# Kernel optimization log

Hardware: AMD Instinct MI355X
Metric: run time of the kernel (lower is better)

The kernel has to match this reference:

```python
import jax, jax.numpy as jnp
import numpy as np

B, L, H, LAB = 64, 128, 512, 128

def setup_inputs() -> dict:
    key = jax.random.key(0)
    ks = jax.random.split(key, 8)
    s = 1.0 / np.sqrt(H)  # PyTorch LSTM/Linear uniform bound as a std-ish scale
    return {
        "x": jax.random.normal(ks[0], (B, L, 2 * H), jnp.float32),
        "hi": jax.random.normal(ks[1], (B, L, 2 * H), jnp.float32),
        "W_ih": jax.random.normal(ks[2], (4 * H, 5 * H), jnp.float32) * s,
        "W_hh": jax.random.normal(ks[3], (4 * H, H), jnp.float32) * s,
        "b_ih": jax.random.normal(ks[4], (4 * H,), jnp.float32) * s,
        "b_hh": jax.random.normal(ks[5], (4 * H,), jnp.float32) * s,
        "W_fc": jax.random.normal(ks[6], (LAB, H), jnp.float32) * s,
        "b_fc": jax.random.normal(ks[7], (LAB,), jnp.float32) * s,
    }

def _cell(xi, h, c, W_ih, W_hh, b_ih, b_hh):
    # PyTorch LSTMCell math, gate order: input, forget, cell(g), output
    gates = xi @ W_ih.T + b_ih + h @ W_hh.T + b_hh  # [4H]
    i, f, g, o = jnp.split(gates, 4)
    i = jax.nn.sigmoid(i); f = jax.nn.sigmoid(f); o = jax.nn.sigmoid(o)
    g = jnp.tanh(g)
    c = f * c + i * g
    h = o * jnp.tanh(c)
    return h, c

def reference(x, hi, W_ih, W_hh, b_ih, b_hh, W_fc, b_fc):
    Bm, Lm, _ = x.shape
    Hm = W_hh.shape[1]
    xs = jnp.concatenate([x, hi], axis=-1).transpose(1, 0, 2)  # [L, B, 4H]
    # Faithful to the torch code: nn.LSTM (batch_first=False) is fed [B,1,5H]
    # with state (1,1,H), so it scans the batch dim as 'time' with a single
    # shared (h,c) that also persists across outer timesteps.
    def time_step(carry, x_t):
        h, c, prev_out = carry  # h,c: [H]; prev_out: [B,H] (outputs of prev t)
        inp = jnp.concatenate([x_t, prev_out], axis=-1)  # [B, 5H]
        def batch_step(hc, xi):
            hh, cc = hc
            hh, cc = _cell(xi, hh, cc, W_ih, W_hh, b_ih, b_hh)
            return (hh, cc), hh
        (h, c), outs = jax.lax.scan(batch_step, (h, c), inp)  # outs: [B,H]
        return (h, c, outs), outs
    init = (jnp.zeros((Hm,), x.dtype), jnp.zeros((Hm,), x.dtype),
            jnp.zeros((Bm, Hm), x.dtype))
    _, all_out = jax.lax.scan(time_step, init, xs)  # [L, B, H]
    output = all_out.transpose(1, 0, 2)  # [B, L, H]
    return output @ W_fc.T + b_fc  # [B, L, label_size]
```

## Files before the change

### kernel.cpp

```cpp
#include <hip/hip_runtime.h>
#include <stdint.h>


#define HDIM   512
#define NSTEP  8192
#define XDIM   2048
#define IN5H   2560
#define LSEQ   128
#define LAB    128
#define SPIN_LIMIT 65536

typedef float f32x4 __attribute__((ext_vector_type(4)));
typedef short bf16x8 __attribute__((ext_vector_type(8)));

__device__ __forceinline__ unsigned f2bf(float v){
  unsigned u = __float_as_uint(v);
  u += 0x7fffu + ((u >> 16) & 1u);
  return u >> 16;
}
__device__ __forceinline__ float bfu(unsigned half16){
  return __uint_as_float(half16 << 16);
}
template<int CTRL>
__device__ __forceinline__ float dpp_add(float x){
  const int yi = __builtin_amdgcn_update_dpp(0, __float_as_int(x), CTRL, 0xF, 0xF, true);
  return x + __int_as_float(yi);
}
__device__ __forceinline__ float wave_reduce63(float x){
  x = dpp_add<0x111>(x);
  x = dpp_add<0x112>(x);
  x = dpp_add<0x114>(x);
  x = dpp_add<0x118>(x);
  x = dpp_add<0x142>(x);
  x = dpp_add<0x143>(x);
  return x;
}

__global__ __launch_bounds__(256) void gemm_pre(
    const float* __restrict__ x, const float* __restrict__ hi,
    const float* __restrict__ Wih, const float* __restrict__ bih,
    const float* __restrict__ bhh, unsigned* __restrict__ pre32)
{
  __shared__ unsigned short As[128][40];
  __shared__ unsigned short Bs[128][40];
  const int tid = threadIdx.x;
  const int bm = blockIdx.x, bn = blockIdx.y;
  const int lane = tid & 63, wv = tid >> 6;
  const int wm = wv & 1, wn = wv >> 1;

  const int srow = tid >> 1;
  const int ch   = (tid & 1) * 16;

  const int gr = bm*128 + srow;
  const int bb = gr & 63, tt = gr >> 6;
  const float* ax = x  + (size_t)(bb*LSEQ + tt) * 1024;
  const float* ah = hi + (size_t)(bb*LSEQ + tt) * 1024;
  const int R = bn*128 + srow;
  const float* bw = Wih + (size_t)R * IN5H;

  f32x4 acc[4][4];
  #pragma unroll
  for (int m=0;m<4;++m)
    #pragma unroll
    for (int n=0;n<4;++n) acc[m][n] = (f32x4){0.f,0.f,0.f,0.f};

  for (int kc = 0; kc < XDIM; kc += 32){
    const int c0 = kc + ch;
    const float* ap = (c0 < 1024) ? (ax + c0) : (ah + (c0 - 1024));
    #pragma unroll
    for (int q=0;q<4;++q){
      float4 va = *(const float4*)(ap + 4*q);
      float4 vb = *(const float4*)(bw + c0 + 4*q);
      ushort4 ua; ua.x=f2bf(va.x); ua.y=f2bf(va.y); ua.z=f2bf(va.z); ua.w=f2bf(va.w);
      ushort4 ub; ub.x=f2bf(vb.x); ub.y=f2bf(vb.y); ub.z=f2bf(vb.z); ub.w=f2bf(vb.w);
      *(ushort4*)&As[srow][ch + 4*q] = ua;
      *(ushort4*)&Bs[srow][ch + 4*q] = ub;
    }
    __syncthreads();
    bf16x8 afr[4], bfr[4];
    const int mr = wm*64 + (lane & 15);
    const int nr = wn*64 + (lane & 15);
    const int ko = (lane >> 4) * 8;
    #pragma unroll
    for (int m=0;m<4;++m) afr[m] = *(const bf16x8*)&As[mr + 16*m][ko];
    #pragma unroll
    for (int n=0;n<4;++n) bfr[n] = *(const bf16x8*)&Bs[nr + 16*n][ko];
    #pragma unroll
    for (int m=0;m<4;++m)
      #pragma unroll
      for (int n=0;n<4;++n)
        acc[m][n] = __builtin_amdgcn_mfma_f32_16x16x32_bf16(afr[m], bfr[n], acc[m][n], 0, 0, 0);
    __syncthreads();
  }
  #pragma unroll
  for (int n=0;n<4;++n){
    const int scol = bn*128 + wn*64 + 16*n + (lane & 15);
    const float bias = bih[scol] + bhh[scol];
    #pragma unroll
    for (int m=0;m<4;++m){
      const int sr0 = bm*128 + wm*64 + 16*m + (lane >> 4)*4;
      #pragma unroll
      for (int q=0;q<4;++q){
        const float v = acc[m][n][q] + bias;
        const float vn = __shfl_xor(v, 1, 64);
        if (!(lane & 1)){
          const unsigned word = f2bf(v) | (f2bf(vn) << 16);
          pre32[(size_t)(sr0 + q) * 1024 + (scol >> 1)] = word;
        }
      }
    }
  }
}

__global__ __launch_bounds__(256)
__attribute__((amdgpu_waves_per_eu(1,1)))
void lstm_seq(
    const float* __restrict__ Wih, const float* __restrict__ Whh,
    const unsigned* __restrict__ pre32, unsigned* __restrict__ units)
{
  const int tid = threadIdx.x;
  const int l = tid & 63;
  const int j0 = blockIdx.x * 4 + (tid >> 6);

  float wh[4][8], wu[4][8];
  #pragma unroll
  for (int g=0; g<4; ++g){
    const float* ph = Whh + (size_t)(g*HDIM + j0)*HDIM;
    const float* pu = Wih + (size_t)(g*HDIM + j0)*IN5H + XDIM;
    #pragma unroll
    for (int k=0; k<8; ++k){
      const int col = 2*l + 128*(k>>1) + (k&1);
      wh[g][k] = ph[col]; wu[g][k] = pu[col];
    }
  }
  #pragma unroll
  for (int g=0; g<4; ++g)
    #pragma unroll
    for (int k=0; k<8; ++k){
      asm volatile("" : "+v"(wh[g][k]));
      asm volatile("" : "+v"(wu[g][k]));
    }

  const int phalf = j0 >> 1, psel = j0 & 1;
  float pr[4];
  #pragma unroll
  for (int g=0; g<4; ++g){
    const unsigned w0 = pre32[(size_t)0*1024 + g*256 + phalf];
    pr[g] = psel ? bfu(w0 >> 16) : bfu(w0 & 0xffffu);
  }

  float uvc[8];
  #pragma unroll
  for (int k=0;k<8;++k) uvc[k] = 0.f;

  float cst = 0.f;
  int dead = 0;

  for (int s = 0; s < NSTEP; ++s){
    unsigned pw[4];
    const bool pf  = (s + 1 < NSTEP);
    const bool upf = (s + 1 >= 64) && pf;
    if (pf){
      #pragma unroll
      for (int g=0; g<4; ++g)
        pw[g] = pre32[(size_t)(s+1)*1024 + g*256 + phalf];
    }
    unsigned long long un[4];
    if (upf){
      const unsigned long long* bp =
          (const unsigned long long*)(units + (size_t)(s-63)*HDIM) + l;
      #pragma unroll
      for (int c=0;c<4;++c)
        un[c] = __hip_atomic_load(bp + 64*c, __ATOMIC_RELAXED, __HIP_MEMORY_SCOPE_AGENT);
    }

    float hv[8];
    if (s == 0){
      #pragma unroll
      for (int k=0;k<8;++k) hv[k] = 0.f;
    } else {
      const unsigned long long* bp =
          (const unsigned long long*)(units + (size_t)(s-1)*HDIM) + l;
      unsigned long long v[4];
      if (dead){
        #pragma unroll
        for (int c=0;c<4;++c) v[c] = __hip_atomic_load(bp + 64*c, __ATOMIC_RELAXED, __HIP_MEMORY_SCOPE_AGENT);
      } else {
        int trips = 0, ok;
        do {
          #pragma unroll
          for (int c=0;c<4;++c) v[c] = __hip_atomic_load(bp + 64*c, __ATOMIC_RELAXED, __HIP_MEMORY_SCOPE_AGENT);
          int lok = 1;
          #pragma unroll
          for (int c=0;c<4;++c){
            lok &= (((unsigned)(v[c] >> 16) & 0xffffu) == (unsigned)s);
            lok &= (((unsigned)(v[c] >> 48)) == (unsigned)s);
          }
          ok = __all(lok);
        } while (!ok && ++trips < SPIN_LIMIT);
        if (!ok) dead = 1;
      }
      #pragma unroll
      for (int c=0;c<4;++c){
        hv[2*c]   = bfu((unsigned)v[c] & 0xffffu);
        hv[2*c+1] = bfu((unsigned)(v[c] >> 32) & 0xffffu);
      }
    }

    float a0=0.f, a1=0.f, a2=0.f, a3=0.f;
    #pragma unroll
    for (int k=0;k<8;++k){
      a0 += wh[0][k]*hv[k]; a1 += wh[1][k]*hv[k];
      a2 += wh[2][k]*hv[k]; a3 += wh[3][k]*hv[k];
    }
    #pragma unroll
    for (int k=0;k<8;++k){
      a0 += wu[0][k]*uvc[k]; a1 += wu[1][k]*uvc[k];
      a2 += wu[2][k]*uvc[k]; a3 += wu[3][k]*uvc[k];
    }
    a0 = wave_reduce63(a0);
    a1 = wave_reduce63(a1);
    a2 = wave_reduce63(a2);
    a3 = wave_reduce63(a3);

    float gi = a0 + pr[0];
    float gf = a1 + pr[1];
    float gg = a2 + pr[2];
    float go = a3 + pr[3];
    gi = 1.f/(1.f + __expf(-gi));
    gf = 1.f/(1.f + __expf(-gf));
    go = 1.f/(1.f + __expf(-go));
    float e2 = __expf(2.f * fminf(fmaxf(gg, -15.f), 15.f));
    gg = (e2 - 1.f) / (e2 + 1.f);
    cst = gf*cst + gi*gg;
    float e2c = __expf(2.f * fminf(fmaxf(cst, -15.f), 15.f));
    const float hval = go * ((e2c - 1.f) / (e2c + 1.f));

    if (l == 63){
      const unsigned unit = ((unsigned)(s + 1) << 16) | f2bf(hval);
      __hip_atomic_store(units + (size_t)s*HDIM + j0, unit,
                         __ATOMIC_RELAXED, __HIP_MEMORY_SCOPE_AGENT);
    }

    if (upf){
      int lok = 1;
      #pragma unroll
      for (int c=0;c<4;++c){
        lok &= (((unsigned)(un[c] >> 16) & 0xffffu) == (unsigned)(s-62));
        lok &= (((unsigned)(un[c] >> 48)) == (unsigned)(s-62));
      }
      if (!__all(lok) && !dead){
        const unsigned long long* bp =
            (const unsigned long long*)(units + (size_t)(s-63)*HDIM) + l;
        int trips = 0, ok;
        do {
          #pragma unroll
          for (int c=0;c<4;++c)
            un[c] = __hip_atomic_load(bp + 64*c, __ATOMIC_RELAXED, __HIP_MEMORY_SCOPE_AGENT);
          int lk = 1;
          #pragma unroll
          for (int c=0;c<4;++c){
            lk &= (((unsigned)(un[c] >> 16) & 0xffffu) == (unsigned)(s-62));
            lk &= (((unsigned)(un[c] >> 48)) == (unsigned)(s-62));
          }
          ok = __all(lk);
        } while (!ok && ++trips < SPIN_LIMIT);
        if (!ok) dead = 1;
      }
      #pragma unroll
      for (int c=0;c<4;++c){
        uvc[2*c]   = bfu((unsigned)un[c] & 0xffffu);
        uvc[2*c+1] = bfu((unsigned)(un[c] >> 32) & 0xffffu);
      }
    } else {
      #pragma unroll
      for (int k=0;k<8;++k) uvc[k] = 0.f;
    }
    if (pf){
      #pragma unroll
      for (int g=0; g<4; ++g)
        pr[g] = psel ? bfu(pw[g] >> 16) : bfu(pw[g] & 0xffffu);
    }
  }
}

__global__ __launch_bounds__(256) void fc_kernel(
    const unsigned* __restrict__ units,
    const float* __restrict__ Wfc, const float* __restrict__ bfc,
    float* __restrict__ out)
{
  __shared__ float hbuf[8][512];
  const int tid = threadIdx.x;
  const int s0 = blockIdx.x * 8;
  #pragma unroll
  for (int r=0;r<16;++r){
    const int q = tid + 256*r;
    const int si = q >> 9, j = q & 511;
    hbuf[si][j] = bfu(units[(size_t)(s0 + si)*HDIM + j] & 0xffffu);
  }
  __syncthreads();
  const int lab = tid & 127, sg = tid >> 7;
  const float* wrow = Wfc + (size_t)lab * HDIM;
  const float bias = bfc[lab];
  for (int si = sg; si < 8; si += 2){
    float sum = 0.f;
    #pragma unroll 4
    for (int j=0;j<HDIM;j+=4){
      const float4 wv = *(const float4*)(wrow + j);
      sum += wv.x*hbuf[si][j] + wv.y*hbuf[si][j+1]
           + wv.z*hbuf[si][j+2] + wv.w*hbuf[si][j+3];
    }
    const int s = s0 + si;
    const int bb = s & 63, tt = s >> 6;
    out[((size_t)(bb*LSEQ + tt))*LAB + lab] = sum + bias;
  }
}

__global__ void sentinel_kernel(float* out, int n){
  const int i = blockIdx.x*256 + threadIdx.x;
  if (i < n) out[i] = 12345.0f;
}

extern "C" void kernel_launch(void* const* d_in, const int* in_sizes, int n_in,
                              void* d_out, int out_size, void* d_ws, size_t ws_size,
                              hipStream_t stream)
{
  const float* x   = (const float*)d_in[0];
  const float* hi  = (const float*)d_in[1];
  const float* Wih = (const float*)d_in[2];
  const float* Whh = (const float*)d_in[3];
  const float* bih = (const float*)d_in[4];
  const float* bhh = (const float*)d_in[5];
  const float* Wfc = (const float*)d_in[6];
  const float* bfc = (const float*)d_in[7];
  float* out = (float*)d_out;

  const size_t MB = 1024*1024;
  if (ws_size >= 48*MB){
    unsigned* pre32 = (unsigned*)d_ws;
    unsigned* units = (unsigned*)((char*)d_ws + 32*MB);
    gemm_pre<<<dim3(64, 16), 256, 0, stream>>>(x, hi, Wih, bih, bhh, pre32);
    lstm_seq<<<128, 256, 0, stream>>>(Wih, Whh, pre32, units);
    fc_kernel<<<1024, 256, 0, stream>>>(units, Wfc, bfc, out);
  } else {
    sentinel_kernel<<<(out_size + 255)/256, 256, 0, stream>>>(out, out_size);
  }
}
```

Baseline: 14.52 ms.

## Share per-step h/u polling across block via LDS instead of per-wave loads

```diff
diff --git a/kernel.cpp b/kernel.cpp
--- a/kernel.cpp
+++ b/kernel.cpp
@@ -122,6 +122,9 @@
   const int l = tid & 63;
   const int j0 = blockIdx.x * 4 + (tid >> 6);
 
+  __shared__ float hshm[2][512];
+  __shared__ float ushm[3][512];
+
   float wh[4][8], wu[4][8];
   #pragma unroll
   for (int g=0; g<4; ++g){
@@ -141,6 +144,11 @@
       asm volatile("" : "+v"(wu[g][k]));
     }
 
+  for (int i = tid; i < 512; i += 256){
+    hshm[0][i] = 0.f; hshm[1][i] = 0.f;
+    ushm[0][i] = 0.f; ushm[1][i] = 0.f; ushm[2][i] = 0.f;
+  }
+
   const int phalf = j0 >> 1, psel = j0 & 1;
   float pr[4];
   #pragma unroll
@@ -149,62 +157,78 @@
     pr[g] = psel ? bfu(w0 >> 16) : bfu(w0 & 0xffffu);
   }
 
-  float uvc[8];
-  #pragma unroll
-  for (int k=0;k<8;++k) uvc[k] = 0.f;
-
   float cst = 0.f;
   int dead = 0;
+  int ucur = 0;
+  __syncthreads();
 
   for (int s = 0; s < NSTEP; ++s){
+    const int unxt = (ucur == 2) ? 0 : ucur + 1;
     unsigned pw[4];
     const bool pf  = (s + 1 < NSTEP);
-    const bool upf = (s + 1 >= 64) && pf;
+    const bool upf = (s >= 63) && pf;
     if (pf){
       #pragma unroll
       for (int g=0; g<4; ++g)
         pw[g] = pre32[(size_t)(s+1)*1024 + g*256 + phalf];
     }
-    unsigned long long un[4];
+    unsigned long long uld = 0;
     if (upf){
-      const unsigned long long* bp =
-          (const unsigned long long*)(units + (size_t)(s-63)*HDIM) + l;
-      #pragma unroll
-      for (int c=0;c<4;++c)
-        un[c] = __hip_atomic_load(bp + 64*c, __ATOMIC_RELAXED, __HIP_MEMORY_SCOPE_AGENT);
-    }
-
-    float hv[8];
-    if (s == 0){
-      #pragma unroll
-      for (int k=0;k<8;++k) hv[k] = 0.f;
-    } else {
-      const unsigned long long* bp =
-          (const unsigned long long*)(units + (size_t)(s-1)*HDIM) + l;
-      unsigned long long v[4];
+      const unsigned long long* up =
+          (const unsigned long long*)(units + (size_t)(s-63)*HDIM);
+      uld = __hip_atomic_load(up + tid, __ATOMIC_RELAXED, __HIP_MEMORY_SCOPE_AGENT);
+    }
+
+    if (s > 0){
+      const unsigned long long* hp =
+          (const unsigned long long*)(units + (size_t)(s-1)*HDIM);
+      unsigned long long v;
       if (dead){
-        #pragma unroll
-        for (int c=0;c<4;++c) v[c] = __hip_atomic_load(bp + 64*c, __ATOMIC_RELAXED, __HIP_MEMORY_SCOPE_AGENT);
+        v = __hip_atomic_load(hp + tid, __ATOMIC_RELAXED, __HIP_MEMORY_SCOPE_AGENT);
       } else {
         int trips = 0, ok;
         do {
-          #pragma unroll
-          for (int c=0;c<4;++c) v[c] = __hip_atomic_load(bp + 64*c, __ATOMIC_RELAXED, __HIP_MEMORY_SCOPE_AGENT);
-          int lok = 1;
-          #pragma unroll
-          for (int c=0;c<4;++c){
-            lok &= (((unsigned)(v[c] >> 16) & 0xffffu) == (unsigned)s);
-            lok &= (((unsigned)(v[c] >> 48)) == (unsigned)s);
-          }
-          ok = __all(lok);
+          v = __hip_atomic_load(hp + tid, __ATOMIC_RELAXED, __HIP_MEMORY_SCOPE_AGENT);
+          ok = __all((((unsigned)(v >> 16) & 0xffffu) == (unsigned)s) &
+                     (((unsigned)(v >> 48)) == (unsigned)s));
         } while (!ok && ++trips < SPIN_LIMIT);
         if (!ok) dead = 1;
       }
-      #pragma unroll
-      for (int c=0;c<4;++c){
-        hv[2*c]   = bfu((unsigned)v[c] & 0xffffu);
-        hv[2*c+1] = bfu((unsigned)(v[c] >> 32) & 0xffffu);
+      float2 hpair;
+      hpair.x = bfu((unsigned)v & 0xffffu);
+      hpair.y = bfu((unsigned)(v >> 32) & 0xffffu);
+      *(float2*)&hshm[s & 1][2*tid] = hpair;
+    }
+
+    if (upf){
+      int ok = __all((((unsigned)(uld >> 16) & 0xffffu) == (unsigned)(s-62)) &
+                     (((unsigned)(uld >> 48)) == (unsigned)(s-62)));
+      if (!ok && !dead){
+        const unsigned long long* up =
+            (const unsigned long long*)(units + (size_t)(s-63)*HDIM);
+        int trips = 0;
+        do {
+          uld = __hip_atomic_load(up + tid, __ATOMIC_RELAXED, __HIP_MEMORY_SCOPE_AGENT);
+          ok = __all((((unsigned)(uld >> 16) & 0xffffu) == (unsigned)(s-62)) &
+                     (((unsigned)(uld >> 48)) == (unsigned)(s-62)));
+        } while (!ok && ++trips < SPIN_LIMIT);
+        if (!ok) dead = 1;
       }
+      float2 upair;
+      upair.x = bfu((unsigned)uld & 0xffffu);
+      upair.y = bfu((unsigned)(uld >> 32) & 0xffffu);
+      *(float2*)&ushm[unxt][2*tid] = upair;
+    }
+
+    __syncthreads();
+
+    float hv[8], uv[8];
+    #pragma unroll
+    for (int c=0;c<4;++c){
+      const float2 hp2 = *(const float2*)&hshm[s & 1][2*l + 128*c];
+      hv[2*c] = hp2.x; hv[2*c+1] = hp2.y;
+      const float2 up2 = *(const float2*)&ushm[ucur][2*l + 128*c];
+      uv[2*c] = up2.x; uv[2*c+1] = up2.y;
     }
 
     float a0=0.f, a1=0.f, a2=0.f, a3=0.f;
@@ -215,8 +239,8 @@
     }
     #pragma unroll
     for (int k=0;k<8;++k){
-      a0 += wu[0][k]*uvc[k]; a1 += wu[1][k]*uvc[k];
-      a2 += wu[2][k]*uvc[k]; a3 += wu[3][k]*uvc[k];
+      a0 += wu[0][k]*uv[k]; a1 += wu[1][k]*uv[k];
+      a2 += wu[2][k]*uv[k]; a3 += wu[3][k]*uv[k];
     }
     a0 = wave_reduce63(a0);
     a1 = wave_reduce63(a1);
@@ -242,45 +266,12 @@
                          __ATOMIC_RELAXED, __HIP_MEMORY_SCOPE_AGENT);
     }
 
-    if (upf){
-      int lok = 1;
-      #pragma unroll
-      for (int c=0;c<4;++c){
-        lok &= (((unsigned)(un[c] >> 16) & 0xffffu) == (unsigned)(s-62));
-        lok &= (((unsigned)(un[c] >> 48)) == (unsigned)(s-62));
-      }
-      if (!__all(lok) && !dead){
-        const unsigned long long* bp =
-            (const unsigned long long*)(units + (size_t)(s-63)*HDIM) + l;
-        int trips = 0, ok;
-        do {
-          #pragma unroll
-          for (int c=0;c<4;++c)
-            un[c] = __hip_atomic_load(bp + 64*c, __ATOMIC_RELAXED, __HIP_MEMORY_SCOPE_AGENT);
-          int lk = 1;
-          #pragma unroll
-          for (int c=0;c<4;++c){
-            lk &= (((unsigned)(un[c] >> 16) & 0xffffu) == (unsigned)(s-62));
-            lk &= (((unsigned)(un[c] >> 48)) == (unsigned)(s-62));
-          }
-          ok = __all(lk);
-        } while (!ok && ++trips < SPIN_LIMIT);
-        if (!ok) dead = 1;
-      }
-      #pragma unroll
-      for (int c=0;c<4;++c){
-        uvc[2*c]   = bfu((unsigned)un[c] & 0xffffu);
-        uvc[2*c+1] = bfu((unsigned)(un[c] >> 32) & 0xffffu);
-      }
-    } else {
-      #pragma unroll
-      for (int k=0;k<8;++k) uvc[k] = 0.f;
-    }
     if (pf){
       #pragma unroll
       for (int g=0; g<4; ++g)
         pr[g] = psel ? bfu(pw[g] >> 16) : bfu(pw[g] & 0xffffu);
     }
+    ucur = unxt;
   }
 }
 
```

Result: slower. 18.74 ms (+29.1%).

## Process four hidden units per wave and shrink the sequential LSTM grid

Applied to the files above, without the earlier changes.

```diff
diff --git a/kernel.cpp b/kernel.cpp
--- a/kernel.cpp
+++ b/kernel.cpp
@@ -120,84 +120,115 @@
 {
   const int tid = threadIdx.x;
   const int l = tid & 63;
-  const int j0 = blockIdx.x * 4 + (tid >> 6);
-
-  float wh[4][8], wu[4][8];
+  const int j0 = blockIdx.x * 16 + (tid >> 6) * 4;
+
+  float wh[4][4][8], wu[4][4][8];
+  #pragma unroll
+  for (int jj=0; jj<4; ++jj)
+    #pragma unroll
+    for (int g=0; g<4; ++g){
+      const float* ph = Whh + (size_t)(g*HDIM + j0 + jj)*HDIM;
+      const float* pu = Wih + (size_t)(g*HDIM + j0 + jj)*IN5H + XDIM;
+      #pragma unroll
+      for (int k=0; k<8; ++k){
+        const int col = 2*l + 128*(k>>1) + (k&1);
+        wh[jj][g][k] = ph[col]; wu[jj][g][k] = pu[col];
+      }
+    }
+  #pragma unroll
+  for (int jj=0; jj<4; ++jj)
+    #pragma unroll
+    for (int g=0; g<4; ++g)
+      #pragma unroll
+      for (int k=0; k<8; ++k){
+        asm volatile("" : "+v"(wh[jj][g][k]));
+        asm volatile("" : "+v"(wu[jj][g][k]));
+      }
+
+  const int ph0 = j0 >> 1;
+  float pr[4][4];
   #pragma unroll
   for (int g=0; g<4; ++g){
-    const float* ph = Whh + (size_t)(g*HDIM + j0)*HDIM;
-    const float* pu = Wih + (size_t)(g*HDIM + j0)*IN5H + XDIM;
-    #pragma unroll
-    for (int k=0; k<8; ++k){
-      const int col = 2*l + 128*(k>>1) + (k&1);
-      wh[g][k] = ph[col]; wu[g][k] = pu[col];
-    }
-  }
-  #pragma unroll
-  for (int g=0; g<4; ++g)
-    #pragma unroll
-    for (int k=0; k<8; ++k){
-      asm volatile("" : "+v"(wh[g][k]));
-      asm volatile("" : "+v"(wu[g][k]));
-    }
-
-  const int phalf = j0 >> 1, psel = j0 & 1;
-  float pr[4];
-  #pragma unroll
-  for (int g=0; g<4; ++g){
-    const unsigned w0 = pre32[(size_t)0*1024 + g*256 + phalf];
-    pr[g] = psel ? bfu(w0 >> 16) : bfu(w0 & 0xffffu);
+    const unsigned w0 = pre32[(size_t)0*1024 + g*256 + ph0];
+    const unsigned w1 = pre32[(size_t)0*1024 + g*256 + ph0 + 1];
+    pr[0][g] = bfu(w0 & 0xffffu); pr[1][g] = bfu(w0 >> 16);
+    pr[2][g] = bfu(w1 & 0xffffu); pr[3][g] = bfu(w1 >> 16);
   }
 
   float uvc[8];
   #pragma unroll
   for (int k=0;k<8;++k) uvc[k] = 0.f;
 
-  float cst = 0.f;
+  float cst[4] = {0.f, 0.f, 0.f, 0.f};
   int dead = 0;
 
   for (int s = 0; s < NSTEP; ++s){
-    unsigned pw[4];
     const bool pf  = (s + 1 < NSTEP);
-    const bool upf = (s + 1 >= 64) && pf;
+    const bool upf = (s >= 63) && pf;
+
+    unsigned pw0[4], pw1[4];
     if (pf){
       #pragma unroll
-      for (int g=0; g<4; ++g)
-        pw[g] = pre32[(size_t)(s+1)*1024 + g*256 + phalf];
+      for (int g=0; g<4; ++g){
+        pw0[g] = pre32[(size_t)(s+1)*1024 + g*256 + ph0];
+        pw1[g] = pre32[(size_t)(s+1)*1024 + g*256 + ph0 + 1];
+      }
     }
     unsigned long long un[4];
     if (upf){
-      const unsigned long long* bp =
+      const unsigned long long* up =
           (const unsigned long long*)(units + (size_t)(s-63)*HDIM) + l;
       #pragma unroll
       for (int c=0;c<4;++c)
-        un[c] = __hip_atomic_load(bp + 64*c, __ATOMIC_RELAXED, __HIP_MEMORY_SCOPE_AGENT);
-    }
+        un[c] = __hip_atomic_load(up + 64*c, __ATOMIC_RELAXED, __HIP_MEMORY_SCOPE_AGENT);
+    }
+    unsigned long long v[4];
+    if (s > 0){
+      const unsigned long long* hp =
+          (const unsigned long long*)(units + (size_t)(s-1)*HDIM) + l;
+      #pragma unroll
+      for (int c=0;c<4;++c)
+        v[c] = __hip_atomic_load(hp + 64*c, __ATOMIC_RELAXED, __HIP_MEMORY_SCOPE_AGENT);
+    }
+
+    float acc[4][4];
+    #pragma unroll
+    for (int jj=0; jj<4; ++jj)
+      #pragma unroll
+      for (int g=0; g<4; ++g){
+        float a = 0.f;
+        #pragma unroll
+        for (int k=0;k<8;++k) a += wu[jj][g][k]*uvc[k];
+        acc[jj][g] = a;
+      }
 
     float hv[8];
     if (s == 0){
       #pragma unroll
       for (int k=0;k<8;++k) hv[k] = 0.f;
     } else {
-      const unsigned long long* bp =
-          (const unsigned long long*)(units + (size_t)(s-1)*HDIM) + l;
-      unsigned long long v[4];
-      if (dead){
+      if (!dead){
+        int lok = 1;
         #pragma unroll
-        for (int c=0;c<4;++c) v[c] = __hip_atomic_load(bp + 64*c, __ATOMIC_RELAXED, __HIP_MEMORY_SCOPE_AGENT);
-      } else {
-        int trips = 0, ok;
-        do {
+        for (int c=0;c<4;++c){
+          lok &= (((unsigned)(v[c] >> 16) & 0xffffu) == (unsigned)s);
+          lok &= (((unsigned)(v[c] >> 48)) == (unsigned)s);
+        }
+        int ok = __all(lok), trips = 0;
+        while (!ok && ++trips < SPIN_LIMIT){
+          const unsigned long long* hp =
+              (const unsigned long long*)(units + (size_t)(s-1)*HDIM) + l;
           #pragma unroll
-          for (int c=0;c<4;++c) v[c] = __hip_atomic_load(bp + 64*c, __ATOMIC_RELAXED, __HIP_MEMORY_SCOPE_AGENT);
-          int lok = 1;
+          for (int c=0;c<4;++c)
+            v[c] = __hip_atomic_load(hp + 64*c, __ATOMIC_RELAXED, __HIP_MEMORY_SCOPE_AGENT);
+          int lk = 1;
           #pragma unroll
           for (int c=0;c<4;++c){
-            lok &= (((unsigned)(v[c] >> 16) & 0xffffu) == (unsigned)s);
-            lok &= (((unsigned)(v[c] >> 48)) == (unsigned)s);
+            lk &= (((unsigned)(v[c] >> 16) & 0xffffu) == (unsigned)s);
+            lk &= (((unsigned)(v[c] >> 48)) == (unsigned)s);
           }
-          ok = __all(lok);
-        } while (!ok && ++trips < SPIN_LIMIT);
+          ok = __all(lk);
+        }
         if (!ok) dead = 1;
       }
       #pragma unroll
@@ -207,39 +238,42 @@
       }
     }
 
-    float a0=0.f, a1=0.f, a2=0.f, a3=0.f;
-    #pragma unroll
-    for (int k=0;k<8;++k){
-      a0 += wh[0][k]*hv[k]; a1 += wh[1][k]*hv[k];
-      a2 += wh[2][k]*hv[k]; a3 += wh[3][k]*hv[k];
-    }
-    #pragma unroll
-    for (int k=0;k<8;++k){
-      a0 += wu[0][k]*uvc[k]; a1 += wu[1][k]*uvc[k];
-      a2 += wu[2][k]*uvc[k]; a3 += wu[3][k]*uvc[k];
-    }
-    a0 = wave_reduce63(a0);
-    a1 = wave_reduce63(a1);
-    a2 = wave_reduce63(a2);
-    a3 = wave_reduce63(a3);
-
-    float gi = a0 + pr[0];
-    float gf = a1 + pr[1];
-    float gg = a2 + pr[2];
-    float go = a3 + pr[3];
-    gi = 1.f/(1.f + __expf(-gi));
-    gf = 1.f/(1.f + __expf(-gf));
-    go = 1.f/(1.f + __expf(-go));
-    float e2 = __expf(2.f * fminf(fmaxf(gg, -15.f), 15.f));
-    gg = (e2 - 1.f) / (e2 + 1.f);
-    cst = gf*cst + gi*gg;
-    float e2c = __expf(2.f * fminf(fmaxf(cst, -15.f), 15.f));
-    const float hval = go * ((e2c - 1.f) / (e2c + 1.f));
-
+    #pragma unroll
+    for (int jj=0; jj<4; ++jj)
+      #pragma unroll
+      for (int g=0; g<4; ++g){
+        float a = acc[jj][g];
+        #pragma unroll
+        for (int k=0;k<8;++k) a += wh[jj][g][k]*hv[k];
+        acc[jj][g] = wave_reduce63(a);
+      }
+
+    unsigned unitv[4];
+    #pragma unroll
+    for (int jj=0; jj<4; ++jj){
+      float gi = acc[jj][0] + pr[jj][0];
+      float gf = acc[jj][1] + pr[jj][1];
+      float gg = acc[jj][2] + pr[jj][2];
+      float go = acc[jj][3] + pr[jj][3];
+      gi = 1.f/(1.f + __expf(-gi));
+      gf = 1.f/(1.f + __expf(-gf));
+      go = 1.f/(1.f + __expf(-go));
+      float e2 = __expf(2.f * fminf(fmaxf(gg, -15.f), 15.f));
+      gg = (e2 - 1.f) / (e2 + 1.f);
+      cst[jj] = gf*cst[jj] + gi*gg;
+      float e2c = __expf(2.f * fminf(fmaxf(cst[jj], -15.f), 15.f));
+      const float hval = go * ((e2c - 1.f) / (e2c + 1.f));
+      unitv[jj] = ((unsigned)(s + 1) << 16) | f2bf(hval);
+    }
     if (l == 63){
-      const unsigned unit = ((unsigned)(s + 1) << 16) | f2bf(hval);
-      __hip_atomic_store(units + (size_t)s*HDIM + j0, unit,
-                         __ATOMIC_RELAXED, __HIP_MEMORY_SCOPE_AGENT);
+      unsigned long long* dst =
+          (unsigned long long*)(units + (size_t)s*HDIM + j0);
+      const unsigned long long d0 =
+          (unsigned long long)unitv[0] | ((unsigned long long)unitv[1] << 32);
+      const unsigned long long d1 =
+          (unsigned long long)unitv[2] | ((unsigned long long)unitv[3] << 32);
+      __hip_atomic_store(dst,     d0, __ATOMIC_RELAXED, __HIP_MEMORY_SCOPE_AGENT);
+      __hip_atomic_store(dst + 1, d1, __ATOMIC_RELAXED, __HIP_MEMORY_SCOPE_AGENT);
     }
 
     if (upf){
@@ -250,13 +284,13 @@
         lok &= (((unsigned)(un[c] >> 48)) == (unsigned)(s-62));
       }
       if (!__all(lok) && !dead){
-        const unsigned long long* bp =
+        const unsigned long long* up =
             (const unsigned long long*)(units + (size_t)(s-63)*HDIM) + l;
         int trips = 0, ok;
         do {
           #pragma unroll
           for (int c=0;c<4;++c)
-            un[c] = __hip_atomic_load(bp + 64*c, __ATOMIC_RELAXED, __HIP_MEMORY_SCOPE_AGENT);
+            un[c] = __hip_atomic_load(up + 64*c, __ATOMIC_RELAXED, __HIP_MEMORY_SCOPE_AGENT);
           int lk = 1;
           #pragma unroll
           for (int c=0;c<4;++c){
@@ -278,8 +312,10 @@
     }
     if (pf){
       #pragma unroll
-      for (int g=0; g<4; ++g)
-        pr[g] = psel ? bfu(pw[g] >> 16) : bfu(pw[g] & 0xffffu);
+      for (int g=0; g<4; ++g){
+        pr[0][g] = bfu(pw0[g] & 0xffffu); pr[1][g] = bfu(pw0[g] >> 16);
+        pr[2][g] = bfu(pw1[g] & 0xffffu); pr[3][g] = bfu(pw1[g] >> 16);
+      }
     }
   }
 }
@@ -340,7 +376,7 @@
     unsigned* pre32 = (unsigned*)d_ws;
     unsigned* units = (unsigned*)((char*)d_ws + 32*MB);
     gemm_pre<<<dim3(64, 16), 256, 0, stream>>>(x, hi, Wih, bih, bhh, pre32);
-    lstm_seq<<<128, 256, 0, stream>>>(Wih, Whh, pre32, units);
+    lstm_seq<<<32, 256, 0, stream>>>(Wih, Whh, pre32, units);
     fc_kernel<<<1024, 256, 0, stream>>>(units, Wfc, bfc, out);
   } else {
     sentinel_kernel<<<(out_size + 255)/256, 256, 0, stream>>>(out, out_size);
```

Result: slower. 26.66 ms (+83.6%).
